# Kernel optimization log

Measured on AMD Instinct MI355X. Metric: run time of the kernel, lower is better.

The kernel has to match this reference:

```python
import jax, jax.numpy as jnp
import numpy as np

N, E, D = 50000, 600000, 128  # nodes, edges, units (== vert_dim, so no W_adapt)


def glorot(key, shape):
    lim = np.sqrt(6.0 / (shape[0] + shape[1]))
    return jax.random.uniform(key, shape, jnp.float32, -lim, lim)


def setup_inputs() -> dict:
    key = jax.random.key(0)
    ks = jax.random.split(key, 8)
    X = jax.random.normal(ks[0], (N, D), jnp.float32)
    ref_a = jax.random.randint(ks[1], (E,), 0, N, jnp.int32)
    ref_b = jax.random.randint(ks[2], (E,), 0, N, jnp.int32)
    # msg_net: two Dense(D) layers, inner_activation=None (linear)
    W1 = glorot(ks[3], (D, D)); b1 = jnp.zeros((D,), jnp.float32)
    W2 = glorot(ks[4], (D, D)); b2 = jnp.zeros((D,), jnp.float32)
    # keras GRUCell (reset_after=True): kernel [D,3D], recurrent_kernel [D,3D], bias [2,3D]
    gru_kernel = glorot(ks[5], (D, 3 * D))
    gru_rkernel = glorot(ks[6], (D, 3 * D))
    gru_bias = jnp.zeros((2, 3 * D), jnp.float32)
    return {"X": X, "ref_a": ref_a, "ref_b": ref_b,
            "W1": W1, "b1": b1, "W2": W2, "b2": b2,
            "gru_kernel": gru_kernel, "gru_rkernel": gru_rkernel, "gru_bias": gru_bias}


def _ggnn(X, ref_a, ref_b, W1, b1, W2, b2, gru_kernel, gru_rkernel, gru_bias):
    # msg_net (depth=2, linear inner activation)
    X_msg = (X @ W1 + b1) @ W2 + b2                       # [N, D]
    # wl1_convolution, undirected: scatter-add both directions
    agg = jnp.zeros_like(X_msg)
    agg = agg.at[ref_b].add(X_msg[ref_a])                 # a -> b
    agg = agg.at[ref_a].add(X_msg[ref_b])                 # b -> a (directed=False)
    # keras GRUCell update: inputs = agg, state = X  (reset_after=True)
    mx = agg @ gru_kernel + gru_bias[0]                   # [N, 3D]
    mh = X @ gru_rkernel + gru_bias[1]                    # [N, 3D]
    xz, xr, xh = jnp.split(mx, 3, axis=-1)
    rz, rr, rh = jnp.split(mh, 3, axis=-1)
    z = jax.nn.sigmoid(xz + rz)
    r = jax.nn.sigmoid(xr + rr)
    hh = jnp.tanh(xh + r * rh)
    return z * X + (1.0 - z) * hh                         # [N, D]


def reference(X, ref_a, ref_b, W1, b1, W2, b2, gru_kernel, gru_rkernel, gru_bias):
    return _ggnn(X, ref_a, ref_b, W1, b1, W2, b2, gru_kernel, gru_rkernel, gru_bias)
```

## Files before the change

### kernel.cpp

```cpp
#include <hip/hip_runtime.h>
#include <cstdint>
#include <cstddef>

typedef __bf16 bf16x8 __attribute__((ext_vector_type(8)));
typedef float  f32x4  __attribute__((ext_vector_type(4)));
typedef short  s16x8  __attribute__((ext_vector_type(8)));

static __device__ __forceinline__ float bf2f(short s) {
    union { unsigned u; float f; } v;
    v.u = ((unsigned)(unsigned short)s) << 16;
    return v.f;
}
static __device__ __forceinline__ short f2bf(float f) {
    unsigned u = __float_as_uint(f);
    u += 0x7fffu + ((u >> 16) & 1u);
    return (short)(u >> 16);
}
static __device__ __forceinline__ float sigmoid_(float x) {
    return 1.0f / (1.0f + __expf(-x));
}
static __device__ __forceinline__ float tanh_(float x) {
    float ax = fabsf(x);
    float e  = __expf(-2.0f * ax);
    float t  = (1.0f - e) / (1.0f + e);
    return copysignf(t, x);
}

#define MFMA(a, b, c) __builtin_amdgcn_mfma_f32_16x16x32_bf16((a), (b), (c), 0, 0, 0)

static __device__ __forceinline__ int lidx8(int r, int ch) {
    return r * 128 + ((ch ^ (r & 15)) << 3);
}
static __device__ __forceinline__ int lidx(int r, int col) {
    return r * 128 + ((((col >> 3) ^ (r & 15)) << 3) | (col & 7));
}

#define BLOCKS1     256
#define STRIPE_CAP  64
#define BUCKET_REG  (BLOCKS1 * STRIPE_CAP)
#define NODE_CAP    96

static __device__ __forceinline__ s16x8 cvt8(const float* p) {
    f32x4 a0 = *(const f32x4*)(p);
    f32x4 a1 = *(const f32x4*)(p + 4);
    s16x8 v;
    v[0] = f2bf(a0[0]); v[1] = f2bf(a0[1]); v[2] = f2bf(a0[2]); v[3] = f2bf(a0[3]);
    v[4] = f2bf(a1[0]); v[5] = f2bf(a1[1]); v[6] = f2bf(a1[2]); v[7] = f2bf(a1[3]);
    return v;
}

__global__ __launch_bounds__(256) void prep_kernel(
    const int* __restrict__ ra, const int* __restrict__ rb,
    unsigned* __restrict__ bucketed, int* __restrict__ stripeCnt,
    int E, int CPB, int nbuckets,
    const float* __restrict__ W1, const float* __restrict__ W2,
    const float* __restrict__ GK, const float* __restrict__ GR,
    short* __restrict__ W1t, short* __restrict__ W2t,
    short* __restrict__ GKt, short* __restrict__ GRt)
{
    __shared__ int cnt[256];
    cnt[threadIdx.x] = 0;

    int i = blockIdx.x * 256 + threadIdx.x;
    if (i < 16384) {
        int k = i >> 7, n = i & 127;
        W1t[n * 128 + k] = f2bf(W1[i]);
        W2t[n * 128 + k] = f2bf(W2[i]);
    }
    if (i < 49152) {
        int k = i / 384, n = i - k * 384;
        GKt[n * 128 + k] = f2bf(GK[i]);
        GRt[n * 128 + k] = f2bf(GR[i]);
    }
    __syncthreads();

    const int blk = blockIdx.x;
    const int e1 = min(E, (blk + 1) * CPB);
    for (int e = blk * CPB + threadIdx.x; e < e1; e += 256) {
        int a = ra[e], b = rb[e];
        int ka = a >> 8, kb = b >> 8;
        int r1 = atomicAdd(&cnt[ka], 1);
        if (r1 < STRIPE_CAP)
            bucketed[(size_t)ka * BUCKET_REG + blk * STRIPE_CAP + r1] =
                ((unsigned)(a & 255) << 16) | (unsigned)b;
        int r2 = atomicAdd(&cnt[kb], 1);
        if (r2 < STRIPE_CAP)
            bucketed[(size_t)kb * BUCKET_REG + blk * STRIPE_CAP + r2] =
                ((unsigned)(b & 255) << 16) | (unsigned)a;
    }
    __syncthreads();
    if ((int)threadIdx.x < nbuckets)
        stripeCnt[(size_t)threadIdx.x * BLOCKS1 + blk] =
            min(cnt[threadIdx.x], STRIPE_CAP);
}

__global__ __launch_bounds__(512) void msg_pass2_kernel(
    const float* __restrict__ X, const short* __restrict__ W1t,
    const float* __restrict__ b1, const short* __restrict__ W2t,
    const float* __restrict__ b2, short* __restrict__ msg, int N, int nblk64,
    const unsigned* __restrict__ bucketed, const int* __restrict__ stripeCnt,
    unsigned short* __restrict__ nbrS, int* __restrict__ counts)
{
    __shared__ short ldsA[64 * 128];
    __shared__ short ldsY[64 * 128];
    __shared__ int off[256];
    __shared__ int scnt[256];
    const int tid = threadIdx.x;

    if ((int)blockIdx.x >= nblk64) {
        const int k = blockIdx.x - nblk64;
        if (tid < 256) {
            off[tid]  = 0;
            scnt[tid] = stripeCnt[(size_t)k * BLOCKS1 + tid];
        }
        __syncthreads();
        const int lo = k << 8;
        const unsigned* reg = bucketed + (size_t)k * BUCKET_REG;
        for (int i = tid; i < BUCKET_REG; i += 512) {
            int blk = i >> 6, slot = i & (STRIPE_CAP - 1);
            if (slot < scnt[blk]) {
                unsigned e = reg[i];
                int nl = (int)(e >> 16);
                int p  = (int)(e & 0xffffu);
                int r  = atomicAdd(&off[nl], 1);
                if (r < NODE_CAP)
                    nbrS[(size_t)(lo + nl) * NODE_CAP + r] = (unsigned short)p;
            }
        }
        __syncthreads();
        int node = lo + tid;
        if (tid < 256 && node < N) counts[node] = min(off[tid], NODE_CAP);
        return;
    }

    const int m0   = blockIdx.x * 64;
    const int lane = tid & 63, wv = tid >> 6;
    const int q = lane >> 4, c = lane & 15;
    const int ncol = wv * 16 + c;

    bf16x8 w1f[4], w2f[4];
#pragma unroll
    for (int ks = 0; ks < 4; ks++) {
        int ko = ks * 32 + q * 8;
        w1f[ks] = __builtin_bit_cast(bf16x8, *(const s16x8*)(W1t + (size_t)ncol * 128 + ko));
        w2f[ks] = __builtin_bit_cast(bf16x8, *(const s16x8*)(W2t + (size_t)ncol * 128 + ko));
    }

    for (int i = tid; i < 64 * 16; i += 512) {
        int r = i >> 4, ch = i & 15;
        s16x8 v;
        if (m0 + r < N) v = cvt8(X + (size_t)(m0 + r) * 128 + ch * 8);
        else            v = (s16x8)0;
        *(s16x8*)(ldsA + lidx8(r, ch)) = v;
    }
    __syncthreads();

    f32x4 acc[4];
#pragma unroll
    for (int rt = 0; rt < 4; rt++) acc[rt] = (f32x4)0.0f;
#pragma unroll
    for (int ks = 0; ks < 4; ks++) {
        int kc = ks * 4 + q;
#pragma unroll
        for (int rt = 0; rt < 4; rt++) {
            bf16x8 aA = __builtin_bit_cast(bf16x8, *(const s16x8*)(ldsA + lidx8(rt * 16 + c, kc)));
            acc[rt] = MFMA(aA, w1f[ks], acc[rt]);
        }
    }
    float bias1 = b1[ncol];
#pragma unroll
    for (int rt = 0; rt < 4; rt++)
#pragma unroll
        for (int i = 0; i < 4; i++)
            ldsY[lidx(rt * 16 + q * 4 + i, ncol)] = f2bf(acc[rt][i] + bias1);
    __syncthreads();

#pragma unroll
    for (int rt = 0; rt < 4; rt++) acc[rt] = (f32x4)0.0f;
#pragma unroll
    for (int ks = 0; ks < 4; ks++) {
        int kc = ks * 4 + q;
#pragma unroll
        for (int rt = 0; rt < 4; rt++) {
            bf16x8 aY = __builtin_bit_cast(bf16x8, *(const s16x8*)(ldsY + lidx8(rt * 16 + c, kc)));
            acc[rt] = MFMA(aY, w2f[ks], acc[rt]);
        }
    }
    float bias2 = b2[ncol];
#pragma unroll
    for (int rt = 0; rt < 4; rt++)
#pragma unroll
        for (int i = 0; i < 4; i++) {
            int row = m0 + rt * 16 + q * 4 + i;
            if (row < N) msg[(size_t)row * 128 + ncol] = f2bf(acc[rt][i] + bias2);
        }
}

__global__ __launch_bounds__(256) void gather_kernel(
    const short* __restrict__ msg, const unsigned short* __restrict__ nbrS,
    const int* __restrict__ counts, short* __restrict__ aggb, int N)
{
    const int lane = threadIdx.x & 63;
    const int node = blockIdx.x * 4 + (threadIdx.x >> 6);
    if (node >= N) return;
    const int g  = lane >> 4;
    const int cl = lane & 15;
    const int s   = node * NODE_CAP;
    const int end = s + counts[node];

    float a[8];
#pragma unroll
    for (int t = 0; t < 8; t++) a[t] = 0.0f;

    int i = s + g;
    for (; i + 12 < end; i += 16) {
        int j0 = (int)nbrS[i];
        int j1 = (int)nbrS[i + 4];
        int j2 = (int)nbrS[i + 8];
        int j3 = (int)nbrS[i + 12];
        s16x8 p0 = *(const s16x8*)(msg + (size_t)j0 * 128 + cl * 8);
        s16x8 p1 = *(const s16x8*)(msg + (size_t)j1 * 128 + cl * 8);
        s16x8 p2 = *(const s16x8*)(msg + (size_t)j2 * 128 + cl * 8);
        s16x8 p3 = *(const s16x8*)(msg + (size_t)j3 * 128 + cl * 8);
#pragma unroll
        for (int t = 0; t < 8; t++) a[t] += bf2f(p0[t]);
#pragma unroll
        for (int t = 0; t < 8; t++) a[t] += bf2f(p1[t]);
#pragma unroll
        for (int t = 0; t < 8; t++) a[t] += bf2f(p2[t]);
#pragma unroll
        for (int t = 0; t < 8; t++) a[t] += bf2f(p3[t]);
    }
    for (; i + 4 < end; i += 8) {
        int j0 = (int)nbrS[i];
        int j1 = (int)nbrS[i + 4];
        s16x8 p0 = *(const s16x8*)(msg + (size_t)j0 * 128 + cl * 8);
        s16x8 p1 = *(const s16x8*)(msg + (size_t)j1 * 128 + cl * 8);
#pragma unroll
        for (int t = 0; t < 8; t++) a[t] += bf2f(p0[t]);
#pragma unroll
        for (int t = 0; t < 8; t++) a[t] += bf2f(p1[t]);
    }
    if (i < end) {
        int j = (int)nbrS[i];
        s16x8 p = *(const s16x8*)(msg + (size_t)j * 128 + cl * 8);
#pragma unroll
        for (int t = 0; t < 8; t++) a[t] += bf2f(p[t]);
    }

#pragma unroll
    for (int t = 0; t < 8; t++) {
        a[t] += __shfl_xor(a[t], 32);
        a[t] += __shfl_xor(a[t], 16);
    }
    if (g == 0) {
        s16x8 o;
#pragma unroll
        for (int t = 0; t < 8; t++) o[t] = f2bf(a[t]);
        *(s16x8*)(aggb + (size_t)node * 128 + cl * 8) = o;
    }
}

__global__ __launch_bounds__(512) void gru_kernel(
    const short* __restrict__ aggb, const float* __restrict__ X,
    const short* __restrict__ GKt, const short* __restrict__ GRt,
    const float* __restrict__ gbias, float* __restrict__ out, int N)
{
    __shared__ short ldsA[64 * 128];
    __shared__ short ldsX[64 * 128];
    const int tid  = threadIdx.x;
    const int m0   = blockIdx.x * 64;
    const int lane = tid & 63, wv = tid >> 6;
    const int q = lane >> 4, c = lane & 15;
    const int ncol = wv * 16 + c;

    bf16x8 bkz[4], bkr[4], bkh[4], brz[4], brr[4], brh[4];
#pragma unroll
    for (int ks = 0; ks < 4; ks++) {
        int ko = ks * 32 + q * 8;
        bkz[ks] = __builtin_bit_cast(bf16x8, *(const s16x8*)(GKt + (size_t)(ncol)       * 128 + ko));
        bkr[ks] = __builtin_bit_cast(bf16x8, *(const s16x8*)(GKt + (size_t)(128 + ncol) * 128 + ko));
        bkh[ks] = __builtin_bit_cast(bf16x8, *(const s16x8*)(GKt + (size_t)(256 + ncol) * 128 + ko));
        brz[ks] = __builtin_bit_cast(bf16x8, *(const s16x8*)(GRt + (size_t)(ncol)       * 128 + ko));
        brr[ks] = __builtin_bit_cast(bf16x8, *(const s16x8*)(GRt + (size_t)(128 + ncol) * 128 + ko));
        brh[ks] = __builtin_bit_cast(bf16x8, *(const s16x8*)(GRt + (size_t)(256 + ncol) * 128 + ko));
    }
    float bz0 = gbias[ncol],       br0 = gbias[128 + ncol],       bh0 = gbias[256 + ncol];
    float bz1 = gbias[384 + ncol], br1 = gbias[384 + 128 + ncol], bh1 = gbias[384 + 256 + ncol];

    for (int i = tid; i < 64 * 16; i += 512) {
        int r = i >> 4, ch = i & 15;
        s16x8 vx, va;
        if (m0 + r < N) {
            vx = cvt8(X + (size_t)(m0 + r) * 128 + ch * 8);
            va = *(const s16x8*)(aggb + (size_t)(m0 + r) * 128 + ch * 8);
        } else { vx = (s16x8)0; va = (s16x8)0; }
        *(s16x8*)(ldsX + lidx8(r, ch)) = vx;
        *(s16x8*)(ldsA + lidx8(r, ch)) = va;
    }
    __syncthreads();

#pragma clang loop unroll(disable)
    for (int rt = 0; rt < 4; rt++) {
        float xv[4];
#pragma unroll
        for (int i = 0; i < 4; i++) {
            int grow = m0 + rt * 16 + q * 4 + i;
            xv[i] = (grow < N) ? X[(size_t)grow * 128 + ncol] : 0.0f;
        }
        f32x4 axz = (f32x4)0.0f, axr = (f32x4)0.0f, axh = (f32x4)0.0f;
        f32x4 arz = (f32x4)0.0f, arr = (f32x4)0.0f, arh = (f32x4)0.0f;
#pragma unroll
        for (int ks = 0; ks < 4; ks++) {
            int kc = ks * 4 + q;
            bf16x8 aA = __builtin_bit_cast(bf16x8, *(const s16x8*)(ldsA + lidx8(rt * 16 + c, kc)));
            bf16x8 aX = __builtin_bit_cast(bf16x8, *(const s16x8*)(ldsX + lidx8(rt * 16 + c, kc)));
            axz = MFMA(aA, bkz[ks], axz);
            axr = MFMA(aA, bkr[ks], axr);
            axh = MFMA(aA, bkh[ks], axh);
            arz = MFMA(aX, brz[ks], arz);
            arr = MFMA(aX, brr[ks], arr);
            arh = MFMA(aX, brh[ks], arh);
        }
#pragma unroll
        for (int i = 0; i < 4; i++) {
            int grow = m0 + rt * 16 + q * 4 + i;
            if (grow < N) {
                float z  = sigmoid_(axz[i] + bz0 + arz[i] + bz1);
                float r  = sigmoid_(axr[i] + br0 + arr[i] + br1);
                float hh = tanh_(axh[i] + bh0 + r * (arh[i] + bh1));
                out[(size_t)grow * 128 + ncol] = z * xv[i] + (1.0f - z) * hh;
            }
        }
    }
}

extern "C" void kernel_launch(void* const* d_in, const int* in_sizes, int n_in,
                              void* d_out, int out_size, void* d_ws, size_t ws_size,
                              hipStream_t stream)
{
    const float* X  = (const float*)d_in[0];
    const int*   ra = (const int*)d_in[1];
    const int*   rb = (const int*)d_in[2];
    const float* W1 = (const float*)d_in[3];
    const float* b1 = (const float*)d_in[4];
    const float* W2 = (const float*)d_in[5];
    const float* b2 = (const float*)d_in[6];
    const float* GK = (const float*)d_in[7];
    const float* GR = (const float*)d_in[8];
    const float* GB = (const float*)d_in[9];
    const int N = in_sizes[0] / 128;
    const int E = in_sizes[1];
    float* out = (float*)d_out;

    const int nbuckets = (N + 255) >> 8;

    char* ws = (char*)d_ws;
    size_t off = 0;
    short* aggb   = (short*)(ws + off);   off += (size_t)N * 128 * 2;
    short* msg    = (short*)(ws + off);   off += (size_t)N * 128 * 2;
    short* W1t    = (short*)(ws + off);   off += 16384u * 2;
    short* W2t    = (short*)(ws + off);   off += 16384u * 2;
    short* GKt    = (short*)(ws + off);   off += 49152u * 2;
    short* GRt    = (short*)(ws + off);   off += 49152u * 2;
    unsigned* bucketed = (unsigned*)(ws + off);
    off += (size_t)nbuckets * BUCKET_REG * 4;
    unsigned short* nbrS = (unsigned short*)(ws + off);
    off += (size_t)nbuckets * 256 * NODE_CAP * 2;
    int* counts    = (int*)(ws + off);    off += (size_t)N * 4;
    int* stripeCnt = (int*)(ws + off);    off += (size_t)nbuckets * BLOCKS1 * 4;

    const int CPB = (E + BLOCKS1 - 1) / BLOCKS1;
    prep_kernel<<<BLOCKS1, 256, 0, stream>>>(ra, rb, bucketed, stripeCnt,
                                             E, CPB, nbuckets,
                                             W1, W2, GK, GR, W1t, W2t, GKt, GRt);

    const int nblk64 = (N + 63) / 64;
    msg_pass2_kernel<<<nblk64 + nbuckets, 512, 0, stream>>>(
        X, W1t, b1, W2t, b2, msg, N, nblk64, bucketed, stripeCnt, nbrS, counts);

    gather_kernel<<<(N + 3) / 4, 256, 0, stream>>>(msg, nbrS, counts, aggb, N);
    gru_kernel<<<nblk64, 512, 0, stream>>>(aggb, X, GKt, GRt, GB, out, N);
}
```

Measured before the change: 203.1 us.

## Fuse neighbor gather into GRU kernel and widen prep blocks

Folds the gather kernel into the GRU kernel: each wave accumulates neighbor messages for 8 rows straight into the LDS A tile, so the bf16 aggregate buffer no longer round-trips through global memory and one launch goes away. The prep kernel moves from 256 to 1024 threads per block, and sigmoid/tanh divides become hardware reciprocal approximations. MFMA sections are wrapped in s_setprio. Risks: the gather now runs on only 782 large blocks, so there is less latency hiding, and the reciprocal approximation loses a little precision.

After: 238.4 us. +17.4%, slower.

```diff
diff --git a/kernel.cpp b/kernel.cpp
--- a/kernel.cpp
+++ b/kernel.cpp
@@ -16,13 +16,16 @@
     u += 0x7fffu + ((u >> 16) & 1u);
     return (short)(u >> 16);
 }
+static __device__ __forceinline__ float rcp_(float x) {
+    return __builtin_amdgcn_rcpf(x);
+}
 static __device__ __forceinline__ float sigmoid_(float x) {
-    return 1.0f / (1.0f + __expf(-x));
+    return rcp_(1.0f + __expf(-x));
 }
 static __device__ __forceinline__ float tanh_(float x) {
     float ax = fabsf(x);
     float e  = __expf(-2.0f * ax);
-    float t  = (1.0f - e) / (1.0f + e);
+    float t  = (1.0f - e) * rcp_(1.0f + e);
     return copysignf(t, x);
 }
 
@@ -49,7 +52,7 @@
     return v;
 }
 
-__global__ __launch_bounds__(256) void prep_kernel(
+__global__ __launch_bounds__(1024) void prep_kernel(
     const int* __restrict__ ra, const int* __restrict__ rb,
     unsigned* __restrict__ bucketed, int* __restrict__ stripeCnt,
     int E, int CPB, int nbuckets,
@@ -59,9 +62,10 @@
     short* __restrict__ GKt, short* __restrict__ GRt)
 {
     __shared__ int cnt[256];
-    cnt[threadIdx.x] = 0;
-
-    int i = blockIdx.x * 256 + threadIdx.x;
+    const int tid = threadIdx.x;
+    if (tid < 256) cnt[tid] = 0;
+
+    int i = blockIdx.x * 1024 + tid;
     if (i < 16384) {
         int k = i >> 7, n = i & 127;
         W1t[n * 128 + k] = f2bf(W1[i]);
@@ -76,7 +80,7 @@
 
     const int blk = blockIdx.x;
     const int e1 = min(E, (blk + 1) * CPB);
-    for (int e = blk * CPB + threadIdx.x; e < e1; e += 256) {
+    for (int e = blk * CPB + tid; e < e1; e += 1024) {
         int a = ra[e], b = rb[e];
         int ka = a >> 8, kb = b >> 8;
         int r1 = atomicAdd(&cnt[ka], 1);
@@ -89,9 +93,9 @@
                 ((unsigned)(b & 255) << 16) | (unsigned)a;
     }
     __syncthreads();
-    if ((int)threadIdx.x < nbuckets)
-        stripeCnt[(size_t)threadIdx.x * BLOCKS1 + blk] =
-            min(cnt[threadIdx.x], STRIPE_CAP);
+    if (tid < nbuckets)
+        stripeCnt[(size_t)tid * BLOCKS1 + blk] =
+            min(cnt[tid], STRIPE_CAP);
 }
 
 __global__ __launch_bounds__(512) void msg_pass2_kernel(
@@ -196,73 +200,9 @@
         }
 }
 
-__global__ __launch_bounds__(256) void gather_kernel(
+__global__ __launch_bounds__(512) void gru_kernel(
     const short* __restrict__ msg, const unsigned short* __restrict__ nbrS,
-    const int* __restrict__ counts, short* __restrict__ aggb, int N)
-{
-    const int lane = threadIdx.x & 63;
-    const int node = blockIdx.x * 4 + (threadIdx.x >> 6);
-    if (node >= N) return;
-    const int g  = lane >> 4;
-    const int cl = lane & 15;
-    const int s   = node * NODE_CAP;
-    const int end = s + counts[node];
-
-    float a[8];
-#pragma unroll
-    for (int t = 0; t < 8; t++) a[t] = 0.0f;
-
-    int i = s + g;
-    for (; i + 12 < end; i += 16) {
-        int j0 = (int)nbrS[i];
-        int j1 = (int)nbrS[i + 4];
-        int j2 = (int)nbrS[i + 8];
-        int j3 = (int)nbrS[i + 12];
-        s16x8 p0 = *(const s16x8*)(msg + (size_t)j0 * 128 + cl * 8);
-        s16x8 p1 = *(const s16x8*)(msg + (size_t)j1 * 128 + cl * 8);
-        s16x8 p2 = *(const s16x8*)(msg + (size_t)j2 * 128 + cl * 8);
-        s16x8 p3 = *(const s16x8*)(msg + (size_t)j3 * 128 + cl * 8);
-#pragma unroll
-        for (int t = 0; t < 8; t++) a[t] += bf2f(p0[t]);
-#pragma unroll
-        for (int t = 0; t < 8; t++) a[t] += bf2f(p1[t]);
-#pragma unroll
-        for (int t = 0; t < 8; t++) a[t] += bf2f(p2[t]);
-#pragma unroll
-        for (int t = 0; t < 8; t++) a[t] += bf2f(p3[t]);
-    }
-    for (; i + 4 < end; i += 8) {
-        int j0 = (int)nbrS[i];
-        int j1 = (int)nbrS[i + 4];
-        s16x8 p0 = *(const s16x8*)(msg + (size_t)j0 * 128 + cl * 8);
-        s16x8 p1 = *(const s16x8*)(msg + (size_t)j1 * 128 + cl * 8);
-#pragma unroll
-        for (int t = 0; t < 8; t++) a[t] += bf2f(p0[t]);
-#pragma unroll
-        for (int t = 0; t < 8; t++) a[t] += bf2f(p1[t]);
-    }
-    if (i < end) {
-        int j = (int)nbrS[i];
-        s16x8 p = *(const s16x8*)(msg + (size_t)j * 128 + cl * 8);
-#pragma unroll
-        for (int t = 0; t < 8; t++) a[t] += bf2f(p[t]);
-    }
-
-#pragma unroll
-    for (int t = 0; t < 8; t++) {
-        a[t] += __shfl_xor(a[t], 32);
-        a[t] += __shfl_xor(a[t], 16);
-    }
-    if (g == 0) {
-        s16x8 o;
-#pragma unroll
-        for (int t = 0; t < 8; t++) o[t] = f2bf(a[t]);
-        *(s16x8*)(aggb + (size_t)node * 128 + cl * 8) = o;
-    }
-}
-
-__global__ __launch_bounds__(512) void gru_kernel(
-    const short* __restrict__ aggb, const float* __restrict__ X,
+    const int* __restrict__ counts, const float* __restrict__ X,
     const short* __restrict__ GKt, const short* __restrict__ GRt,
     const float* __restrict__ gbias, float* __restrict__ out, int N)
 {
@@ -274,6 +214,72 @@
     const int q = lane >> 4, c = lane & 15;
     const int ncol = wv * 16 + c;
 
+    for (int i = tid; i < 64 * 16; i += 512) {
+        int r = i >> 4, ch = i & 15;
+        s16x8 vx;
+        if (m0 + r < N) vx = cvt8(X + (size_t)(m0 + r) * 128 + ch * 8);
+        else            vx = (s16x8)0;
+        *(s16x8*)(ldsX + lidx8(r, ch)) = vx;
+    }
+
+    for (int k = 0; k < 8; k++) {
+        const int r    = wv * 8 + k;
+        const int node = m0 + r;
+        float a[8];
+#pragma unroll
+        for (int t = 0; t < 8; t++) a[t] = 0.0f;
+        if (node < N) {
+            const int s   = node * NODE_CAP;
+            const int end = s + counts[node];
+            int i = s + q;
+            for (; i + 12 < end; i += 16) {
+                int j0 = (int)nbrS[i];
+                int j1 = (int)nbrS[i + 4];
+                int j2 = (int)nbrS[i + 8];
+                int j3 = (int)nbrS[i + 12];
+                s16x8 p0 = *(const s16x8*)(msg + (size_t)j0 * 128 + c * 8);
+                s16x8 p1 = *(const s16x8*)(msg + (size_t)j1 * 128 + c * 8);
+                s16x8 p2 = *(const s16x8*)(msg + (size_t)j2 * 128 + c * 8);
+                s16x8 p3 = *(const s16x8*)(msg + (size_t)j3 * 128 + c * 8);
+#pragma unroll
+                for (int t = 0; t < 8; t++) a[t] += bf2f(p0[t]);
+#pragma unroll
+                for (int t = 0; t < 8; t++) a[t] += bf2f(p1[t]);
+#pragma unroll
+                for (int t = 0; t < 8; t++) a[t] += bf2f(p2[t]);
+#pragma unroll
+                for (int t = 0; t < 8; t++) a[t] += bf2f(p3[t]);
+            }
+            for (; i + 4 < end; i += 8) {
+                int j0 = (int)nbrS[i];
+                int j1 = (int)nbrS[i + 4];
+                s16x8 p0 = *(const s16x8*)(msg + (size_t)j0 * 128 + c * 8);
+                s16x8 p1 = *(const s16x8*)(msg + (size_t)j1 * 128 + c * 8);
+#pragma unroll
+                for (int t = 0; t < 8; t++) a[t] += bf2f(p0[t]);
+#pragma unroll
+                for (int t = 0; t < 8; t++) a[t] += bf2f(p1[t]);
+            }
+            if (i < end) {
+                int j = (int)nbrS[i];
+                s16x8 p = *(const s16x8*)(msg + (size_t)j * 128 + c * 8);
+#pragma unroll
+                for (int t = 0; t < 8; t++) a[t] += bf2f(p[t]);
+            }
+        }
+#pragma unroll
+        for (int t = 0; t < 8; t++) {
+            a[t] += __shfl_xor(a[t], 32);
+            a[t] += __shfl_xor(a[t], 16);
+        }
+        if (q == 0) {
+            s16x8 o;
+#pragma unroll
+            for (int t = 0; t < 8; t++) o[t] = f2bf(a[t]);
+            *(s16x8*)(ldsA + lidx8(r, c)) = o;
+        }
+    }
+
     bf16x8 bkz[4], bkr[4], bkh[4], brz[4], brr[4], brh[4];
 #pragma unroll
     for (int ks = 0; ks < 4; ks++) {
@@ -287,17 +293,6 @@
     }
     float bz0 = gbias[ncol],       br0 = gbias[128 + ncol],       bh0 = gbias[256 + ncol];
     float bz1 = gbias[384 + ncol], br1 = gbias[384 + 128 + ncol], bh1 = gbias[384 + 256 + ncol];
-
-    for (int i = tid; i < 64 * 16; i += 512) {
-        int r = i >> 4, ch = i & 15;
-        s16x8 vx, va;
-        if (m0 + r < N) {
-            vx = cvt8(X + (size_t)(m0 + r) * 128 + ch * 8);
-            va = *(const s16x8*)(aggb + (size_t)(m0 + r) * 128 + ch * 8);
-        } else { vx = (s16x8)0; va = (s16x8)0; }
-        *(s16x8*)(ldsX + lidx8(r, ch)) = vx;
-        *(s16x8*)(ldsA + lidx8(r, ch)) = va;
-    }
     __syncthreads();
 
 #pragma clang loop unroll(disable)
@@ -310,6 +305,7 @@
         }
         f32x4 axz = (f32x4)0.0f, axr = (f32x4)0.0f, axh = (f32x4)0.0f;
         f32x4 arz = (f32x4)0.0f, arr = (f32x4)0.0f, arh = (f32x4)0.0f;
+        __builtin_amdgcn_s_setprio(1);
 #pragma unroll
         for (int ks = 0; ks < 4; ks++) {
             int kc = ks * 4 + q;
@@ -322,6 +318,7 @@
             arr = MFMA(aX, brr[ks], arr);
             arh = MFMA(aX, brh[ks], arh);
         }
+        __builtin_amdgcn_s_setprio(0);
 #pragma unroll
         for (int i = 0; i < 4; i++) {
             int grow = m0 + rt * 16 + q * 4 + i;
@@ -357,7 +354,6 @@
 
     char* ws = (char*)d_ws;
     size_t off = 0;
-    short* aggb   = (short*)(ws + off);   off += (size_t)N * 128 * 2;
     short* msg    = (short*)(ws + off);   off += (size_t)N * 128 * 2;
     short* W1t    = (short*)(ws + off);   off += 16384u * 2;
     short* W2t    = (short*)(ws + off);   off += 16384u * 2;
@@ -371,14 +367,13 @@
     int* stripeCnt = (int*)(ws + off);    off += (size_t)nbuckets * BLOCKS1 * 4;
 
     const int CPB = (E + BLOCKS1 - 1) / BLOCKS1;
-    prep_kernel<<<BLOCKS1, 256, 0, stream>>>(ra, rb, bucketed, stripeCnt,
-                                             E, CPB, nbuckets,
-                                             W1, W2, GK, GR, W1t, W2t, GKt, GRt);
+    prep_kernel<<<BLOCKS1, 1024, 0, stream>>>(ra, rb, bucketed, stripeCnt,
+                                              E, CPB, nbuckets,
+                                              W1, W2, GK, GR, W1t, W2t, GKt, GRt);
 
     const int nblk64 = (N + 63) / 64;
     msg_pass2_kernel<<<nblk64 + nbuckets, 512, 0, stream>>>(
         X, W1t, b1, W2t, b2, msg, N, nblk64, bucketed, stripeCnt, nbrS, counts);
 
-    gather_kernel<<<(N + 3) / 4, 256, 0, stream>>>(msg, nbrS, counts, aggb, N);
-    gru_kernel<<<nblk64, 512, 0, stream>>>(aggb, X, GKt, GRt, GB, out, N);
-}
+    gru_kernel<<<nblk64, 512, 0, stream>>>(msg, nbrS, counts, X, GKt, GRt, GB, out, N);
+}
```

## Overlap edge bucketing with message MLP and split pass2 into own kernel

Applied to the files above, without the earlier changes.

Merges the edge-bucketing pass into the message-MLP launch so the two run as independent block ranges. The second bucketing pass moves into its own small kernel after them. The MLP blocks now read and convert fp32 W1/W2 directly with strided loads, which drops the separate bf16 transpose of those weights. Sigmoid and tanh now use a hardware reciprocal instead of a division. The trade-off is redundant, uncoalesced weight loads in every MLP block, one extra launch, and slightly less precise activations.

Measured after the change: 203.3 us. About the same (+0.1%).

```diff
diff --git a/kernel.cpp b/kernel.cpp
--- a/kernel.cpp
+++ b/kernel.cpp
@@ -16,13 +16,16 @@
     u += 0x7fffu + ((u >> 16) & 1u);
     return (short)(u >> 16);
 }
+static __device__ __forceinline__ float rcp_(float x) {
+    return __builtin_amdgcn_rcpf(x);
+}
 static __device__ __forceinline__ float sigmoid_(float x) {
-    return 1.0f / (1.0f + __expf(-x));
+    return rcp_(1.0f + __expf(-x));
 }
 static __device__ __forceinline__ float tanh_(float x) {
     float ax = fabsf(x);
     float e  = __expf(-2.0f * ax);
-    float t  = (1.0f - e) / (1.0f + e);
+    float t  = (1.0f - e) * rcp_(1.0f + e);
     return copysignf(t, x);
 }
 
@@ -49,91 +52,55 @@
     return v;
 }
 
-__global__ __launch_bounds__(256) void prep_kernel(
+__global__ __launch_bounds__(512) void pass1_msg_kernel(
     const int* __restrict__ ra, const int* __restrict__ rb,
     unsigned* __restrict__ bucketed, int* __restrict__ stripeCnt,
     int E, int CPB, int nbuckets,
-    const float* __restrict__ W1, const float* __restrict__ W2,
     const float* __restrict__ GK, const float* __restrict__ GR,
-    short* __restrict__ W1t, short* __restrict__ W2t,
-    short* __restrict__ GKt, short* __restrict__ GRt)
-{
-    __shared__ int cnt[256];
-    cnt[threadIdx.x] = 0;
-
-    int i = blockIdx.x * 256 + threadIdx.x;
-    if (i < 16384) {
-        int k = i >> 7, n = i & 127;
-        W1t[n * 128 + k] = f2bf(W1[i]);
-        W2t[n * 128 + k] = f2bf(W2[i]);
-    }
-    if (i < 49152) {
-        int k = i / 384, n = i - k * 384;
-        GKt[n * 128 + k] = f2bf(GK[i]);
-        GRt[n * 128 + k] = f2bf(GR[i]);
-    }
-    __syncthreads();
-
-    const int blk = blockIdx.x;
-    const int e1 = min(E, (blk + 1) * CPB);
-    for (int e = blk * CPB + threadIdx.x; e < e1; e += 256) {
-        int a = ra[e], b = rb[e];
-        int ka = a >> 8, kb = b >> 8;
-        int r1 = atomicAdd(&cnt[ka], 1);
-        if (r1 < STRIPE_CAP)
-            bucketed[(size_t)ka * BUCKET_REG + blk * STRIPE_CAP + r1] =
-                ((unsigned)(a & 255) << 16) | (unsigned)b;
-        int r2 = atomicAdd(&cnt[kb], 1);
-        if (r2 < STRIPE_CAP)
-            bucketed[(size_t)kb * BUCKET_REG + blk * STRIPE_CAP + r2] =
-                ((unsigned)(b & 255) << 16) | (unsigned)a;
-    }
-    __syncthreads();
-    if ((int)threadIdx.x < nbuckets)
-        stripeCnt[(size_t)threadIdx.x * BLOCKS1 + blk] =
-            min(cnt[threadIdx.x], STRIPE_CAP);
-}
-
-__global__ __launch_bounds__(512) void msg_pass2_kernel(
-    const float* __restrict__ X, const short* __restrict__ W1t,
-    const float* __restrict__ b1, const short* __restrict__ W2t,
-    const float* __restrict__ b2, short* __restrict__ msg, int N, int nblk64,
-    const unsigned* __restrict__ bucketed, const int* __restrict__ stripeCnt,
-    unsigned short* __restrict__ nbrS, int* __restrict__ counts)
+    short* __restrict__ GKt, short* __restrict__ GRt,
+    const float* __restrict__ X,
+    const float* __restrict__ W1, const float* __restrict__ b1,
+    const float* __restrict__ W2, const float* __restrict__ b2,
+    short* __restrict__ msg, int N)
 {
     __shared__ short ldsA[64 * 128];
     __shared__ short ldsY[64 * 128];
-    __shared__ int off[256];
-    __shared__ int scnt[256];
+    __shared__ int cnt[256];
     const int tid = threadIdx.x;
 
-    if ((int)blockIdx.x >= nblk64) {
-        const int k = blockIdx.x - nblk64;
-        if (tid < 256) {
-            off[tid]  = 0;
-            scnt[tid] = stripeCnt[(size_t)k * BLOCKS1 + tid];
+    if ((int)blockIdx.x < BLOCKS1) {
+        if (tid < 256) cnt[tid] = 0;
+
+        int i = blockIdx.x * 512 + tid;
+        if (i < 49152) {
+            int k = i / 384, n = i - k * 384;
+            GKt[n * 128 + k] = f2bf(GK[i]);
+            GRt[n * 128 + k] = f2bf(GR[i]);
         }
         __syncthreads();
-        const int lo = k << 8;
-        const unsigned* reg = bucketed + (size_t)k * BUCKET_REG;
-        for (int i = tid; i < BUCKET_REG; i += 512) {
-            int blk = i >> 6, slot = i & (STRIPE_CAP - 1);
-            if (slot < scnt[blk]) {
-                unsigned e = reg[i];
-                int nl = (int)(e >> 16);
-                int p  = (int)(e & 0xffffu);
-                int r  = atomicAdd(&off[nl], 1);
-                if (r < NODE_CAP)
-                    nbrS[(size_t)(lo + nl) * NODE_CAP + r] = (unsigned short)p;
-            }
+
+        const int blk = blockIdx.x;
+        const int e1 = min(E, (blk + 1) * CPB);
+        for (int e = blk * CPB + tid; e < e1; e += 512) {
+            int a = ra[e], b = rb[e];
+            int ka = a >> 8, kb = b >> 8;
+            int r1 = atomicAdd(&cnt[ka], 1);
+            if (r1 < STRIPE_CAP)
+                bucketed[(size_t)ka * BUCKET_REG + blk * STRIPE_CAP + r1] =
+                    ((unsigned)(a & 255) << 16) | (unsigned)b;
+            int r2 = atomicAdd(&cnt[kb], 1);
+            if (r2 < STRIPE_CAP)
+                bucketed[(size_t)kb * BUCKET_REG + blk * STRIPE_CAP + r2] =
+                    ((unsigned)(b & 255) << 16) | (unsigned)a;
         }
         __syncthreads();
-        int node = lo + tid;
-        if (tid < 256 && node < N) counts[node] = min(off[tid], NODE_CAP);
+        if (tid < nbuckets)
+            stripeCnt[(size_t)tid * BLOCKS1 + blk] =
+                min(cnt[tid], STRIPE_CAP);
         return;
     }
 
-    const int m0   = blockIdx.x * 64;
+    const int m0   = (blockIdx.x - BLOCKS1) * 64;
     const int lane = tid & 63, wv = tid >> 6;
     const int q = lane >> 4, c = lane & 15;
     const int ncol = wv * 16 + c;
@@ -141,9 +108,15 @@
     bf16x8 w1f[4], w2f[4];
 #pragma unroll
     for (int ks = 0; ks < 4; ks++) {
-        int ko = ks * 32 + q * 8;
-        w1f[ks] = __builtin_bit_cast(bf16x8, *(const s16x8*)(W1t + (size_t)ncol * 128 + ko));
-        w2f[ks] = __builtin_bit_cast(bf16x8, *(const s16x8*)(W2t + (size_t)ncol * 128 + ko));
+        s16x8 v1, v2;
+#pragma unroll
+        for (int t = 0; t < 8; t++) {
+            int k = ks * 32 + q * 8 + t;
+            v1[t] = f2bf(W1[(size_t)k * 128 + ncol]);
+            v2[t] = f2bf(W2[(size_t)k * 128 + ncol]);
+        }
+        w1f[ks] = __builtin_bit_cast(bf16x8, v1);
+        w2f[ks] = __builtin_bit_cast(bf16x8, v2);
     }
 
     for (int i = tid; i < 64 * 16; i += 512) {
@@ -194,6 +167,37 @@
             int row = m0 + rt * 16 + q * 4 + i;
             if (row < N) msg[(size_t)row * 128 + ncol] = f2bf(acc[rt][i] + bias2);
         }
+}
+
+__global__ __launch_bounds__(512) void pass2_kernel(
+    const unsigned* __restrict__ bucketed, const int* __restrict__ stripeCnt,
+    unsigned short* __restrict__ nbrS, int* __restrict__ counts, int N)
+{
+    __shared__ int off[256];
+    __shared__ int scnt[256];
+    const int tid = threadIdx.x;
+    const int k = blockIdx.x;
+    if (tid < 256) {
+        off[tid]  = 0;
+        scnt[tid] = stripeCnt[(size_t)k * BLOCKS1 + tid];
+    }
+    __syncthreads();
+    const int lo = k << 8;
+    const unsigned* reg = bucketed + (size_t)k * BUCKET_REG;
+    for (int i = tid; i < BUCKET_REG; i += 512) {
+        int blk = i >> 6, slot = i & (STRIPE_CAP - 1);
+        if (slot < scnt[blk]) {
+            unsigned e = reg[i];
+            int nl = (int)(e >> 16);
+            int p  = (int)(e & 0xffffu);
+            int r  = atomicAdd(&off[nl], 1);
+            if (r < NODE_CAP)
+                nbrS[(size_t)(lo + nl) * NODE_CAP + r] = (unsigned short)p;
+        }
+    }
+    __syncthreads();
+    int node = lo + tid;
+    if (tid < 256 && node < N) counts[node] = min(off[tid], NODE_CAP);
 }
 
 __global__ __launch_bounds__(256) void gather_kernel(
@@ -359,8 +363,6 @@
     size_t off = 0;
     short* aggb   = (short*)(ws + off);   off += (size_t)N * 128 * 2;
     short* msg    = (short*)(ws + off);   off += (size_t)N * 128 * 2;
-    short* W1t    = (short*)(ws + off);   off += 16384u * 2;
-    short* W2t    = (short*)(ws + off);   off += 16384u * 2;
     short* GKt    = (short*)(ws + off);   off += 49152u * 2;
     short* GRt    = (short*)(ws + off);   off += 49152u * 2;
     unsigned* bucketed = (unsigned*)(ws + off);
@@ -371,14 +373,16 @@
     int* stripeCnt = (int*)(ws + off);    off += (size_t)nbuckets * BLOCKS1 * 4;
 
     const int CPB = (E + BLOCKS1 - 1) / BLOCKS1;
-    prep_kernel<<<BLOCKS1, 256, 0, stream>>>(ra, rb, bucketed, stripeCnt,
-                                             E, CPB, nbuckets,
-                                             W1, W2, GK, GR, W1t, W2t, GKt, GRt);
-
     const int nblk64 = (N + 63) / 64;
-    msg_pass2_kernel<<<nblk64 + nbuckets, 512, 0, stream>>>(
-        X, W1t, b1, W2t, b2, msg, N, nblk64, bucketed, stripeCnt, nbrS, counts);
+
+    pass1_msg_kernel<<<BLOCKS1 + nblk64, 512, 0, stream>>>(
+        ra, rb, bucketed, stripeCnt, E, CPB, nbuckets,
+        GK, GR, GKt, GRt,
+        X, W1, b1, W2, b2, msg, N);
+
+    pass2_kernel<<<nbuckets, 512, 0, stream>>>(bucketed, stripeCnt, nbrS, counts, N);
 
     gather_kernel<<<(N + 3) / 4, 256, 0, stream>>>(msg, nbrS, counts, aggb, N);
+
     gru_kernel<<<nblk64, 512, 0, stream>>>(aggb, X, GKt, GRt, GB, out, N);
 }
```
